# Optimization experiments

Hardware: AMD Instinct MI355X
Metric: run time of the kernel (lower is better)

The kernel has to match this reference:

```python
import jax, jax.numpy as jnp
import numpy as np


def blend_act(x):
    # x>0: 0.9*x + 0.1*tanh(x); else 0.5*tanh(x)
    t = jnp.tanh(x)
    return jnp.where(x > 0, x * 0.9 + t * 0.1, t * 0.5)


def setup_inputs() -> dict:
    key = jax.random.key(0)
    ks = jax.random.split(key, 7)
    B, D_in, H, C = 32768, 512, 1024, 10
    x = jax.random.normal(ks[0], (B, D_in), dtype=jnp.float32)
    s1 = 1.0 / np.sqrt(D_in)
    s2 = 1.0 / np.sqrt(H)
    s3 = 1.0 / np.sqrt(H // 2)
    W1 = jax.random.uniform(ks[1], (D_in, H), jnp.float32, -s1, s1)
    b1 = jax.random.uniform(ks[2], (H,), jnp.float32, -s1, s1)
    W2 = jax.random.uniform(ks[3], (H, H // 2), jnp.float32, -s2, s2)
    b2 = jax.random.uniform(ks[4], (H // 2,), jnp.float32, -s2, s2)
    W3 = jax.random.uniform(ks[5], (H // 2, C), jnp.float32, -s3, s3)
    b3 = jax.random.uniform(ks[6], (C,), jnp.float32, -s3, s3)
    return {"x": x, "W1": W1, "b1": b1, "W2": W2, "b2": b2, "W3": W3, "b3": b3}


def reference(x, W1, b1, W2, b2, W3, b3):
    h = blend_act(x @ W1 + b1)
    # dropout is identity in eval/inference mode
    h = jax.nn.relu(h @ W2 + b2)
    return h @ W3 + b3
```

## Files before the change

kernel.cpp:

```cpp
#include <hip/hip_runtime.h>
#include <hip/hip_bf16.h>
#include <hip/hip_fp16.h>
#include <cstdint>

typedef __attribute__((ext_vector_type(8))) short s16x8;
typedef __attribute__((ext_vector_type(8))) _Float16 f16x8;
typedef __attribute__((ext_vector_type(4))) float f32x4;

__device__ __forceinline__ void gload16(const void* g, void* l){
  __builtin_amdgcn_global_load_lds((const __attribute__((address_space(1))) void*)g,
                                   (__attribute__((address_space(3))) void*)l, 16, 0, 0);
}

__global__ void transpose_f16(const float* __restrict__ in, ushort* __restrict__ outT,
                              int K, int N){
  __shared__ float tile[32][33];
  const int kb = blockIdx.y * 32, nb = blockIdx.x * 32;
  const int tx = threadIdx.x & 31, ty = threadIdx.x >> 5;
#pragma unroll
  for (int r = 0; r < 32; r += 8)
    tile[ty + r][tx] = in[(size_t)(kb + ty + r) * N + nb + tx];
  __syncthreads();
#pragma unroll
  for (int r = 0; r < 32; r += 8){
    const float v = tile[tx][ty + r];
    const _Float16 h = (_Float16)v;
    outT[(size_t)(nb + ty + r) * K + kb + tx] = __builtin_bit_cast(ushort, h);
  }
}

__global__ void finish_out(const float* __restrict__ part, const float* __restrict__ b3,
                           float* __restrict__ out){
  const int idx = blockIdx.x * 256 + threadIdx.x;
  if (idx >= 32768 * 10) return;
  out[idx] = b3[idx % 10] + part[idx] + part[327680 + idx];
}

template<int MODE>
__global__ __launch_bounds__(256, 2)
void gemm_f16_128x256(const void* __restrict__ Asrc, const ushort* __restrict__ Bw,
                      const float* __restrict__ bias, ushort* __restrict__ outH,
                      const float* __restrict__ W3, float* __restrict__ part,
                      int N, int K)
{
  __shared__ ushort lds[MODE == 0 ? 32768 : 36992];
  const int t = threadIdx.x;
  const int lane = t & 63;
  const int wn = t >> 6;
  const int ln15 = lane & 15, lnHi = lane >> 4;

  const int gx = gridDim.x;
  const int nwg = gx * gridDim.y;
  const int bid = blockIdx.y * gx + blockIdx.x;
  const int swz = (bid & 7) * (nwg >> 3) + (bid >> 3);
  const int m0 = (swz / gx) * 128;
  const int n0 = (swz % gx) * 256;

  const ushort* gB = Bw + (size_t)n0 * K;

  if constexpr (MODE == 1){
    ushort* w3lds = &lds[32768];
#pragma unroll
    for (int i2 = 0; i2 < 16; ++i2){
      const int idx = i2 * 256 + t;
      const int c = idx >> 8, k = idx & 255;
      const float v = (c < 10) ? W3[(size_t)(n0 + k) * 10 + c] : 0.f;
      w3lds[c * 264 + k] = __builtin_bit_cast(ushort, (_Float16)v);
    }
  }

  const int rh0  = t >> 3;
  const int slot = t & 7;
  const int gkhw = ((slot << 4) ^ ((rh0 & 7) << 4)) >> 1;
  const uint dA = (uint)(rh0 * 64 + slot * 8);
  const uint dB = (uint)(8192 + rh0 * 64 + slot * 8);
  const ushort* pB = gB + (size_t)rh0 * K + gkhw;
  const float*  pAf = (const float*)Asrc + ((size_t)(m0 + rh0)) * K + slot * 8;
  const uint    dAw = (uint)(rh0 * 64 + ((slot ^ (rh0 & 7)) << 3));
  const ushort* pAh = (const ushort*)Asrc + ((size_t)(m0 + rh0)) * K + gkhw;

  const int swb = (ln15 & 7) << 4;
  const int koff0 = ((lnHi * 16) ^ swb) >> 1;
  const int koff1 = koff0 ^ 32;
  const int hA = ln15 * 64;
  const int hB = 8192 + (wn * 64 + ln15) * 64;

  f32x4 acc[8][4] = {};

  for (int kt = 0; kt < K; kt += 64){
    __syncthreads();
    if constexpr (MODE == 0){
      f32x4 av[4][2];
#pragma unroll
      for (int c = 0; c < 4; ++c){
        const float* src = pAf + (size_t)c * 32 * K + kt;
        av[c][0] = *(const f32x4*)src;
        av[c][1] = *(const f32x4*)(src + 4);
      }
#pragma unroll
      for (int c = 0; c < 8; ++c)
        gload16(pB + (size_t)c * 32 * K + kt, &lds[dB + c * 2048]);
#pragma unroll
      for (int c = 0; c < 4; ++c){
        f16x8 hv;
#pragma unroll
        for (int j = 0; j < 4; ++j){
          hv[j]     = (_Float16)av[c][0][j];
          hv[4 + j] = (_Float16)av[c][1][j];
        }
        *(f16x8*)&lds[dAw + c * 2048] = hv;
      }
    } else {
#pragma unroll
      for (int c = 0; c < 4; ++c)
        gload16(pAh + (size_t)c * 32 * K + kt, &lds[dA + c * 2048]);
#pragma unroll
      for (int c = 0; c < 8; ++c)
        gload16(pB + (size_t)c * 32 * K + kt, &lds[dB + c * 2048]);
    }
    __syncthreads();
    {
      f16x8 af[8], bfv[4];
#pragma unroll
      for (int m = 0; m < 8; ++m)
        af[m] = *(const f16x8*)&lds[hA + m * 1024 + koff0];
#pragma unroll
      for (int j = 0; j < 4; ++j)
        bfv[j] = *(const f16x8*)&lds[hB + j * 1024 + koff0];
      __builtin_amdgcn_s_setprio(1);
#pragma unroll
      for (int m = 0; m < 8; ++m)
#pragma unroll
        for (int j = 0; j < 4; ++j)
          acc[m][j] = __builtin_amdgcn_mfma_f32_16x16x32_f16(af[m], bfv[j], acc[m][j], 0, 0, 0);
      __builtin_amdgcn_s_setprio(0);
    }
    __builtin_amdgcn_sched_barrier(0);
    {
      f16x8 af[8], bfv[4];
#pragma unroll
      for (int m = 0; m < 8; ++m)
        af[m] = *(const f16x8*)&lds[hA + m * 1024 + koff1];
#pragma unroll
      for (int j = 0; j < 4; ++j)
        bfv[j] = *(const f16x8*)&lds[hB + j * 1024 + koff1];
      __builtin_amdgcn_s_setprio(1);
#pragma unroll
      for (int m = 0; m < 8; ++m)
#pragma unroll
        for (int j = 0; j < 4; ++j)
          acc[m][j] = __builtin_amdgcn_mfma_f32_16x16x32_f16(af[m], bfv[j], acc[m][j], 0, 0, 0);
      __builtin_amdgcn_s_setprio(0);
    }
  }

  __syncthreads();

  const int rowbase = lnHi * 4;
  const int colbase = wn * 64 + ln15;
#pragma unroll
  for (int j = 0; j < 4; ++j){
    const int col = colbase + j * 16;
    const float bv = bias[n0 + col];
#pragma unroll
    for (int i = 0; i < 8; ++i){
#pragma unroll
      for (int r = 0; r < 4; ++r){
        const int row = rowbase + i * 16 + r;
        const float v = acc[i][j][r] + bv;
        float a;
        if (MODE == 0){
          const float th = 1.f - 2.f / (__expf(2.f * v) + 1.f);
          a = v > 0.f ? v * 0.9f + th * 0.1f : th * 0.5f;
        } else {
          a = v > 0.f ? v : 0.f;
        }
        const _Float16 h = (_Float16)a;
        lds[row * 256 + (col ^ ((row & 7) << 3))] = __builtin_bit_cast(ushort, h);
      }
    }
  }
  __syncthreads();

  if constexpr (MODE == 0){
#pragma unroll
    for (int it = 0; it < 16; ++it){
      const int chunk = it * 256 + t;
      const int row = chunk >> 5, g = chunk & 31;
      const s16x8 vv = *(const s16x8*)&lds[row * 256 + ((g ^ (row & 7)) << 3)];
      *(s16x8*)&outH[(size_t)(m0 + row) * N + n0 + (g << 3)] = vv;
    }
  } else {
    const ushort* w3lds = &lds[32768];
    const int nb = n0 >> 8;
    f32x4 p3[2] = {};
#pragma unroll
    for (int ks = 0; ks < 8; ++ks){
      const f16x8 bw = *(const f16x8*)&w3lds[ln15 * 264 + ks * 32 + lnHi * 8];
#pragma unroll
      for (int f = 0; f < 2; ++f){
        const int mr = wn * 32 + f * 16 + ln15;
        const int colhw = ks * 32 + lnHi * 8;
        const f16x8 aw = *(const f16x8*)&lds[mr * 256 + (colhw ^ ((mr & 7) << 3))];
        p3[f] = __builtin_amdgcn_mfma_f32_16x16x32_f16(aw, bw, p3[f], 0, 0, 0);
      }
    }
    const int c = ln15;
    if (c < 10){
#pragma unroll
      for (int f = 0; f < 2; ++f)
#pragma unroll
        for (int r = 0; r < 4; ++r){
          const int m = m0 + wn * 32 + f * 16 + lnHi * 4 + r;
          part[((size_t)nb * 32768 + m) * 10 + c] = p3[f][r];
        }
    }
  }
}

extern "C" void kernel_launch(void* const* d_in, const int* in_sizes, int n_in,
                              void* d_out, int out_size, void* d_ws, size_t ws_size,
                              hipStream_t stream){
  const float* x  = (const float*)d_in[0];
  const float* W1 = (const float*)d_in[1];
  const float* b1 = (const float*)d_in[2];
  const float* W2 = (const float*)d_in[3];
  const float* b2 = (const float*)d_in[4];
  const float* W3 = (const float*)d_in[5];
  const float* b3 = (const float*)d_in[6];
  float* out = (float*)d_out;

  const int B = 32768, Din = 512, H = 1024, Hh = 512;
  char* ws = (char*)d_ws;
  const size_t MB = (size_t)1 << 20;
  ushort* h1   = (ushort*)(ws);
  float*  part = (float*)(ws + 64 * MB);
  ushort* W1T  = (ushort*)(ws + 96 * MB);
  ushort* W2T  = (ushort*)(ws + 97 * MB);

  transpose_f16<<<dim3(H / 32, Din / 32), 256, 0, stream>>>(W1, W1T, Din, H);
  transpose_f16<<<dim3(Hh / 32, H / 32), 256, 0, stream>>>(W2, W2T, H, Hh);

  gemm_f16_128x256<0><<<dim3(H / 256, B / 128), 256, 0, stream>>>(
      x,  W1T, b1, h1, nullptr, nullptr, H, Din);
  gemm_f16_128x256<1><<<dim3(Hh / 256, B / 128), 256, 0, stream>>>(
      h1, W2T, b2, nullptr, W3, part, Hh, H);
  finish_out<<<(B * 10 + 255) / 256, 256, 0, stream>>>(part, b3, out);
}
```

Baseline: 115.2 us.

## Split GEMM epilogue into two half-width passes to shrink LDS footprint

The epilogue now stages the 128x256 output tile through LDS in two 128-column halves, and the W3 slice is loaded per half into a smaller pane. This cuts static LDS from 64-72KB to 48KB per block, which could allow more resident workgroups per CU. The cost is an extra pair of barriers, idle waves during each half, and W3 loads moved from the prologue into the epilogue where they are no longer overlapped.

```diff
diff --git a/kernel.cpp b/kernel.cpp
--- a/kernel.cpp
+++ b/kernel.cpp
@@ -43,7 +43,7 @@
                       const float* __restrict__ W3, float* __restrict__ part,
                       int N, int K)
 {
-  __shared__ ushort lds[MODE == 0 ? 32768 : 36992];
+  __shared__ ushort lds[24576];
   const int t = threadIdx.x;
   const int lane = t & 63;
   const int wn = t >> 6;
@@ -57,17 +57,6 @@
   const int n0 = (swz % gx) * 256;
 
   const ushort* gB = Bw + (size_t)n0 * K;
-
-  if constexpr (MODE == 1){
-    ushort* w3lds = &lds[32768];
-#pragma unroll
-    for (int i2 = 0; i2 < 16; ++i2){
-      const int idx = i2 * 256 + t;
-      const int c = idx >> 8, k = idx & 255;
-      const float v = (c < 10) ? W3[(size_t)(n0 + k) * 10 + c] : 0.f;
-      w3lds[c * 264 + k] = __builtin_bit_cast(ushort, (_Float16)v);
-    }
-  }
 
   const int rh0  = t >> 3;
   const int slot = t & 7;
@@ -154,57 +143,75 @@
     }
   }
 
-  __syncthreads();
-
   const int rowbase = lnHi * 4;
-  const int colbase = wn * 64 + ln15;
-#pragma unroll
-  for (int j = 0; j < 4; ++j){
-    const int col = colbase + j * 16;
-    const float bv = bias[n0 + col];
-#pragma unroll
-    for (int i = 0; i < 8; ++i){
-#pragma unroll
-      for (int r = 0; r < 4; ++r){
-        const int row = rowbase + i * 16 + r;
-        const float v = acc[i][j][r] + bv;
-        float a;
-        if (MODE == 0){
-          const float th = 1.f - 2.f / (__expf(2.f * v) + 1.f);
-          a = v > 0.f ? v * 0.9f + th * 0.1f : th * 0.5f;
-        } else {
-          a = v > 0.f ? v : 0.f;
-        }
-        const _Float16 h = (_Float16)a;
-        lds[row * 256 + (col ^ ((row & 7) << 3))] = __builtin_bit_cast(ushort, h);
-      }
-    }
-  }
-  __syncthreads();
-
-  if constexpr (MODE == 0){
-#pragma unroll
-    for (int it = 0; it < 16; ++it){
-      const int chunk = it * 256 + t;
-      const int row = chunk >> 5, g = chunk & 31;
-      const s16x8 vv = *(const s16x8*)&lds[row * 256 + ((g ^ (row & 7)) << 3)];
-      *(s16x8*)&outH[(size_t)(m0 + row) * N + n0 + (g << 3)] = vv;
-    }
-  } else {
-    const ushort* w3lds = &lds[32768];
+  const int colloc  = (wn & 1) * 64 + ln15;
+  const int wnh     = wn >> 1;
+  f32x4 p3[2] = {{0.f,0.f,0.f,0.f},{0.f,0.f,0.f,0.f}};
+
+#pragma unroll
+  for (int p = 0; p < 2; ++p){
+    __syncthreads();
+    if constexpr (MODE == 1){
+      ushort* pane = &lds[16384];
+#pragma unroll
+      for (int i2 = 0; i2 < 8; ++i2){
+        const int idx = i2 * 256 + t;
+        const int c = idx >> 7, k2 = idx & 127;
+        const float v = (c < 10) ? W3[(size_t)(n0 + p * 128 + k2) * 10 + c] : 0.f;
+        pane[c * 136 + k2] = __builtin_bit_cast(ushort, (_Float16)v);
+      }
+    }
+    if (wnh == p){
+#pragma unroll
+      for (int j = 0; j < 4; ++j){
+        const int col = colloc + j * 16;
+        const float bv = bias[n0 + p * 128 + col];
+#pragma unroll
+        for (int i = 0; i < 8; ++i){
+#pragma unroll
+          for (int r = 0; r < 4; ++r){
+            const int row = rowbase + i * 16 + r;
+            const float v = acc[i][j][r] + bv;
+            float a;
+            if (MODE == 0){
+              const float th = 1.f - 2.f / (__expf(2.f * v) + 1.f);
+              a = v > 0.f ? v * 0.9f + th * 0.1f : th * 0.5f;
+            } else {
+              a = v > 0.f ? v : 0.f;
+            }
+            const _Float16 h = (_Float16)a;
+            lds[row * 128 + (col ^ ((row & 7) << 3))] = __builtin_bit_cast(ushort, h);
+          }
+        }
+      }
+    }
+    __syncthreads();
+    if constexpr (MODE == 0){
+#pragma unroll
+      for (int it = 0; it < 8; ++it){
+        const int chunk = it * 256 + t;
+        const int row = chunk >> 4, g = chunk & 15;
+        const s16x8 vv = *(const s16x8*)&lds[row * 128 + ((g ^ (row & 7)) << 3)];
+        *(s16x8*)&outH[(size_t)(m0 + row) * N + n0 + p * 128 + (g << 3)] = vv;
+      }
+    } else {
+      const ushort* pane = &lds[16384];
+#pragma unroll
+      for (int ks = 0; ks < 4; ++ks){
+        const f16x8 bw = *(const f16x8*)&pane[ln15 * 136 + ks * 32 + lnHi * 8];
+#pragma unroll
+        for (int f = 0; f < 2; ++f){
+          const int mr = wn * 32 + f * 16 + ln15;
+          const int colhw = ks * 32 + lnHi * 8;
+          const f16x8 aw = *(const f16x8*)&lds[mr * 128 + (colhw ^ ((mr & 7) << 3))];
+          p3[f] = __builtin_amdgcn_mfma_f32_16x16x32_f16(aw, bw, p3[f], 0, 0, 0);
+        }
+      }
+    }
+  }
+
+  if constexpr (MODE == 1){
     const int nb = n0 >> 8;
-    f32x4 p3[2] = {};
-#pragma unroll
-    for (int ks = 0; ks < 8; ++ks){
-      const f16x8 bw = *(const f16x8*)&w3lds[ln15 * 264 + ks * 32 + lnHi * 8];
-#pragma unroll
-      for (int f = 0; f < 2; ++f){
-        const int mr = wn * 32 + f * 16 + ln15;
-        const int colhw = ks * 32 + lnHi * 8;
-        const f16x8 aw = *(const f16x8*)&lds[mr * 256 + (colhw ^ ((mr & 7) << 3))];
-        p3[f] = __builtin_amdgcn_mfma_f32_16x16x32_f16(aw, bw, p3[f], 0, 0, 0);
-      }
-    }
     const int c = ln15;
     if (c < 10){
 #pragma unroll
```

Result: slower. 132.9 us (+15.4%).
